# Performance work log

Hardware: AMD Instinct MI355X
Metric: run time of the kernel (lower is better)

## Reference

```python
import jax, jax.numpy as jnp
import numpy as np

S, FRAME, CLS, D, HWA, HWV, DOUT = 32, 8, 32, 512, 8, 14, 128


def setup_inputs() -> dict:
    key = jax.random.key(0)
    ks = jax.random.split(key, 12)
    rng = np.random.default_rng(0)
    # per-(segment,class) random permutation of frames (torch.randperm(frame))
    rand_frames = np.stack([rng.permutation(FRAME) for _ in range(S * CLS)]).reshape(S, CLS, FRAME).astype(np.int32)
    rand_classes = rng.integers(0, CLS, size=(S, CLS, FRAME)).astype(np.int32)
    return {
        "feat_a": jax.random.normal(ks[0], (S * CLS, D, HWA, HWA), jnp.float32),
        "pred_a": jax.random.uniform(ks[1], (S, CLS), jnp.float32),
        "feat_v": jax.random.normal(ks[2], (S * FRAME, D, HWV, HWV), jnp.float32),
        "pred_v": jax.random.normal(ks[3], (S * FRAME, CLS), jnp.float32),
        "cam": jax.random.uniform(ks[4], (S * FRAME, CLS, 1, HWV, HWV), jnp.float32),
        "rand_frames": jnp.asarray(rand_frames),
        "rand_classes": jnp.asarray(rand_classes),
        "Wt": jax.random.normal(ks[5], (D, D), jnp.float32) * (1.0 / np.sqrt(D)),
        "bt": jnp.zeros((D,), jnp.float32),
        "Ws": jax.random.normal(ks[6], (D, D), jnp.float32) * (1.0 / np.sqrt(D)),
        "bs": jnp.zeros((D,), jnp.float32),
        "Wa": jax.random.normal(ks[7], (DOUT, D), jnp.float32) * (1.0 / np.sqrt(D)),
        "ba": jnp.zeros((DOUT,), jnp.float32),
        "Wv": jax.random.normal(ks[8], (DOUT, D), jnp.float32) * (1.0 / np.sqrt(D)),
        "bv": jnp.zeros((DOUT,), jnp.float32),
    }


def reference(feat_a, pred_a, feat_v, pred_v, cam, rand_frames, rand_classes,
              Wt, bt, Ws, bs, Wa, ba, Wv, bv):
    S_, C_ = pred_a.shape
    F_ = pred_v.shape[0] // S_

    # temp_conv (1x1) + AdaptiveMaxPool2d(1,1): max over H,W (bias is per-channel const)
    ca = jnp.einsum('bihw,oi->bohw', feat_a, Wt)  # [S*C, D, H, W]
    fa = ca.max(axis=(2, 3)) + bt                 # [S*C, D]
    fa = fa.reshape(S_, C_, -1)                   # [S, C, D]

    # spa_conv (1x1) then cam-weighted foreground pooling (fg branch of cam_pool)
    cv = jnp.einsum('bihw,oi->bohw', feat_v, Ws) + bs[None, :, None, None]  # [S*F, D, H, W]
    camq = cam[:, :, 0]                                                     # [S*F, C, H, W]
    fg = jnp.einsum('bdhw,bchw->bcd', cv, camq)
    fg = fg / (camq.sum(axis=(2, 3))[..., None] + 1e-10)                    # [S*F, C, D]
    fg = fg.reshape(S_, F_, C_, -1)                                         # [S, F, C, D]

    pv = jax.nn.sigmoid(pred_v.reshape(S_, F_, C_))
    active_a = pred_a > 0.3            # [S, C]  (index_a; the chained-index line is a no-op)
    active_v = pv > 0.3                # [S, F, C] (eff_v membership)

    # transforms
    ta = fa @ Wa.T + ba                                    # [S, C, DOUT]
    tv = jnp.einsum('sfcd,od->sfco', fg, Wv) + bv          # [S, F, C, DOUT]

    # 'same' pairs: (seg, frame, class) where both audio class and video frame-class fire
    mask_co = (active_a[:, None, :] & active_v)            # [S, F, C]
    loss_co = ((ta[:, None, :, :] - tv) ** 2).mean(-1)     # [S, F, C]
    loss_co = jnp.transpose(loss_co, (0, 2, 1)) * jnp.transpose(mask_co, (0, 2, 1))  # [S, C, F]

    # 'differ' pairs: num = int(pred_a*frame) random (frame,class) picks from partner seg
    num = (pred_a * F_).astype(jnp.int32)                  # [S, C]
    mask_di = active_a[:, :, None] & (jnp.arange(F_)[None, None, :] < num[:, :, None])  # [S, C, F]
    rank = jnp.arange(S_) ^ 1                              # seg+1 if even else seg-1
    tv_di = tv[rank[:, None, None], rand_frames, rand_classes]  # [S, C, F, DOUT]
    loss_di = ((ta[:, :, None, :] - tv_di) ** 2).mean(-1) * mask_di  # [S, C, F]

    # dense masked layout of (embed_co, embed_di); invalid slots are exactly 0
    return jnp.stack([loss_co, loss_di])  # [2, S, C, F]
```

## Files before the change

kernel.cpp:

```cpp
#include <hip/hip_runtime.h>


typedef __attribute__((ext_vector_type(8))) short bf16x8;
typedef __attribute__((ext_vector_type(4))) float f32x4;

__device__ __forceinline__ unsigned short f2bf(float x) {
    union { float f; unsigned u; } v; v.f = x;
    unsigned r = v.u + 0x7FFFu + ((v.u >> 16) & 1u);
    return (unsigned short)(r >> 16);
}
__device__ __forceinline__ unsigned pk2(float a, float b) {
    return (unsigned)f2bf(a) | ((unsigned)f2bf(b) << 16);
}

__global__ __launch_bounds__(256) void k0_wtf(
    const float* __restrict__ Wt, unsigned short* __restrict__ WtF)
{
    int g = blockIdx.x * 256 + threadIdx.x;
    int ot = g >> 10, ks = (g >> 6) & 15, l = g & 63;
    int lo = l & 15, hi = l >> 4;
    const float* src = &Wt[(ot*16 + lo) * 512 + ks*32 + hi*8];
    float4 f0 = ((const float4*)src)[0], f1 = ((const float4*)src)[1];
    uint4 u = { pk2(f0.x,f0.y), pk2(f0.z,f0.w), pk2(f1.x,f1.y), pk2(f1.z,f1.w) };
    *(uint4*)&WtF[(size_t)g * 8] = u;
}

__global__ __launch_bounds__(512, 4) void k1_fa(
    const float* __restrict__ feat_a, const unsigned short* __restrict__ WtF,
    const float* __restrict__ bt, float* __restrict__ fa)
{
    __shared__ unsigned short lds_b[64 * 512];
    const int b = blockIdx.x, t = threadIdx.x;
    const int w = t >> 6, l = t & 63, lo = l & 15, hi = l >> 4;

    const float* fb = feat_a + (size_t)b * 32768;
    const int hw = l;
#pragma unroll 2
    for (int it = 0; it < 8; ++it) {
        int koct = it * 8 + w;
        float v[8];
#pragma unroll
        for (int j = 0; j < 8; ++j)
            v[j] = fb[(koct * 8 + j) * 64 + hw];
        unsigned u[4];
#pragma unroll
        for (int j = 0; j < 4; ++j) u[j] = pk2(v[2*j], v[2*j + 1]);
        int chunk = koct ^ (hw & 7);
        *(uint4*)((char*)lds_b + hw * 1024 + chunk * 16) = *(uint4*)u;
    }
    __syncthreads();

    f32x4 acc[4][4];
#pragma unroll
    for (int i = 0; i < 4; ++i)
#pragma unroll
        for (int j = 0; j < 4; ++j) acc[i][j] = (f32x4)(0.f);
    const unsigned short* wtf = WtF + (size_t)(w * 4) * 8192;
    for (int ks = 0; ks < 16; ++ks) {
        bf16x8 bfr[4];
#pragma unroll
        for (int nf = 0; nf < 4; ++nf) {
            int chunk = (ks * 4 + hi) ^ (lo & 7);
            bfr[nf] = *(const bf16x8*)((char*)lds_b + (nf*16 + lo) * 1024 + chunk * 16);
        }
#pragma unroll
        for (int mo = 0; mo < 4; ++mo) {
            bf16x8 afr = *(const bf16x8*)&wtf[(size_t)((mo*16 + ks)*64 + l) * 8];
#pragma unroll
            for (int nf = 0; nf < 4; ++nf)
                acc[mo][nf] = __builtin_amdgcn_mfma_f32_16x16x32_bf16(afr, bfr[nf], acc[mo][nf], 0, 0, 0);
        }
    }
    const int o0 = w * 64;
#pragma unroll
    for (int mo = 0; mo < 4; ++mo)
#pragma unroll
        for (int reg = 0; reg < 4; ++reg) {
            float m = fmaxf(fmaxf(acc[mo][0][reg], acc[mo][1][reg]),
                            fmaxf(acc[mo][2][reg], acc[mo][3][reg]));
            m = fmaxf(m, __shfl_xor(m, 1));
            m = fmaxf(m, __shfl_xor(m, 2));
            m = fmaxf(m, __shfl_xor(m, 4));
            m = fmaxf(m, __shfl_xor(m, 8));
            if (lo == 0) {
                int orow = o0 + mo*16 + hi*4 + reg;
                fa[(size_t)b * 512 + orow] = m + bt[orow];
            }
        }
}

__global__ __launch_bounds__(512) void k2_g(
    const float* __restrict__ feat_v, const float* __restrict__ cam,
    unsigned short* __restrict__ g_bf, float* __restrict__ camsum)
{
    __shared__ unsigned short cam_s[32][232];
    __shared__ unsigned short feat_s[2][64][232];
    const int half = blockIdx.x, b = blockIdx.y, t = threadIdx.x;
    const int w = t >> 6, l = t & 63, lo = l & 15, hi = l >> 4;
    const int mo = w >> 2, nf = w & 3;

    const float* camb = &cam[b * 6272];
    for (int i4 = t; i4 < 1568; i4 += 512) {
        int c = i4 / 49, h4 = (i4 - c*49) * 4;
        float4 v = ((const float4*)camb)[i4];
        *(unsigned*)&cam_s[c][h4]     = pk2(v.x, v.y);
        *(unsigned*)&cam_s[c][h4 + 2] = pk2(v.z, v.w);
    }
    for (int idx = t; idx < 32*28; idx += 512) {
        int c = idx / 28; cam_s[c][196 + (idx - c*28)] = 0;
    }
    for (int idx = t; idx < 2*64*28; idx += 512) {
        int bu = idx / 1792, r = (idx - bu*1792) / 28, hh = 196 + (idx % 28);
        feat_s[bu][r][hh] = 0;
    }
    if (half == 0) {
        int c = t >> 4, seg = l & 15;
        int h0 = seg * 13, h1 = min(196, h0 + 13);
        float s = 0.f;
        const float* p = &camb[c * 196];
        for (int q = h0; q < h1; ++q) s += p[q];
        s += __shfl_xor(s, 1); s += __shfl_xor(s, 2);
        s += __shfl_xor(s, 4); s += __shfl_xor(s, 8);
        if (seg == 0) camsum[b*32 + c] = s;
    }

    auto STAGE = [&](int ic, int bu) {
        const float* fbv = &feat_v[((size_t)b*512 + ic*64) * 196];
        for (int i4 = t; i4 < 3136; i4 += 512) {
            int r = i4 / 49, h4 = (i4 - r*49) * 4;
            float4 v = ((const float4*)fbv)[i4];
            *(unsigned*)&feat_s[bu][r][h4]     = pk2(v.x, v.y);
            *(unsigned*)&feat_s[bu][r][h4 + 2] = pk2(v.z, v.w);
        }
    };
    STAGE(half*4, 0);
    __syncthreads();
    for (int q = 0; q < 4; ++q) {
        int ic = half*4 + q;
        if (q < 3) STAGE(ic + 1, (q + 1) & 1);
        f32x4 acc = (f32x4)(0.f);
#pragma unroll
        for (int kt = 0; kt < 7; ++kt) {
            bf16x8 a  = *(const bf16x8*)&cam_s[mo*16 + lo][kt*32 + hi*8];
            bf16x8 bb = *(const bf16x8*)&feat_s[q & 1][nf*16 + lo][kt*32 + hi*8];
            acc = __builtin_amdgcn_mfma_f32_16x16x32_bf16(a, bb, acc, 0, 0, 0);
        }
#pragma unroll
        for (int reg = 0; reg < 4; ++reg) {
            int c = mo*16 + hi*4 + reg;
            int i = ic*64 + nf*16 + lo;
            g_bf[((size_t)b*32 + c)*512 + i] = f2bf(acc[reg]);
        }
        __syncthreads();
    }
}

__global__ __launch_bounds__(256) void k3_wvs(
    const float* __restrict__ Wv, const float* __restrict__ Ws, const float* __restrict__ bs,
    unsigned short* __restrict__ WvsF, float* __restrict__ wvbs)
{
    __shared__ float red[256];
    const int o = blockIdx.x >> 1, ih = blockIdx.x & 1, t = threadIdx.x;
    const int i = ih*256 + t;
    float a0 = 0.f;
#pragma unroll 4
    for (int d = 0; d < 512; ++d)
        a0 += Wv[o*512 + d] * Ws[d*512 + i];
    int nf = o >> 4, lo2 = o & 15, ks = i >> 5, hi2 = (i >> 3) & 3, j = i & 7;
    WvsF[(size_t)(((nf*16 + ks)*64) + hi2*16 + lo2)*8 + j] = f2bf(a0);
    if (ih == 0) {
        red[t] = Wv[o*512 + t]*bs[t] + Wv[o*512 + t + 256]*bs[t + 256];
        __syncthreads();
        for (int s2 = 128; s2 > 0; s2 >>= 1) {
            if (t < s2) red[t] += red[t + s2];
            __syncthreads();
        }
        if (t == 0) wvbs[o] = red[0];
    }
}

__global__ __launch_bounds__(256) void k4_tv(
    const unsigned short* __restrict__ g_bf, const unsigned short* __restrict__ WvsF,
    const float* __restrict__ camsum, const float* __restrict__ wvbs,
    const float* __restrict__ bv, float* __restrict__ tv)
{
    const int m0 = blockIdx.x * 32;
    const int t = threadIdx.x, w = t >> 6, l = t & 63, lo = l & 15, hi = l >> 4;
    f32x4 acc[2][2];
#pragma unroll
    for (int i = 0; i < 2; ++i)
#pragma unroll
        for (int j = 0; j < 2; ++j) acc[i][j] = (f32x4)(0.f);
    for (int ks = 0; ks < 16; ++ks) {
        bf16x8 a0 = *(const bf16x8*)&g_bf[(size_t)(m0 + lo)*512 + ks*32 + hi*8];
        bf16x8 a1 = *(const bf16x8*)&g_bf[(size_t)(m0 + 16 + lo)*512 + ks*32 + hi*8];
#pragma unroll
        for (int nn = 0; nn < 2; ++nn) {
            int nf = w*2 + nn;
            bf16x8 bb = *(const bf16x8*)&WvsF[(size_t)((nf*16 + ks)*64 + l) * 8];
            acc[0][nn] = __builtin_amdgcn_mfma_f32_16x16x32_bf16(a0, bb, acc[0][nn], 0, 0, 0);
            acc[1][nn] = __builtin_amdgcn_mfma_f32_16x16x32_bf16(a1, bb, acc[1][nn], 0, 0, 0);
        }
    }
#pragma unroll
    for (int mo = 0; mo < 2; ++mo)
#pragma unroll
        for (int reg = 0; reg < 4; ++reg) {
            int bc = m0 + mo*16 + hi*4 + reg;
            float cs = camsum[bc];
            float inv = 1.f / (cs + 1e-10f);
#pragma unroll
            for (int nn = 0; nn < 2; ++nn) {
                int o = (w*2 + nn)*16 + lo;
                tv[(size_t)bc*128 + o] = (acc[mo][nn][reg] + cs * wvbs[o]) * inv + bv[o];
            }
        }
}

__global__ __launch_bounds__(128) void k5_ta(
    const float* __restrict__ fa, const float* __restrict__ Wa,
    const float* __restrict__ ba, float* __restrict__ ta)
{
    __shared__ float fa_s[4 * 512];
    const int r0 = blockIdx.x * 4, t = threadIdx.x;
    for (int j = t; j < 512; j += 128)
        ((float4*)fa_s)[j] = ((const float4*)&fa[r0 * 512])[j];
    __syncthreads();
    float acc[4];
#pragma unroll
    for (int r = 0; r < 4; ++r) acc[r] = 0.f;
    const float4* wa4 = (const float4*)&Wa[t * 512];
#pragma unroll 4
    for (int j = 0; j < 128; ++j) {
        float4 wv = wa4[j];
#pragma unroll
        for (int r = 0; r < 4; ++r) {
            float4 fv = ((const float4*)&fa_s[r * 512])[j];
            acc[r] += wv.x*fv.x + wv.y*fv.y + wv.z*fv.z + wv.w*fv.w;
        }
    }
    float bao = ba[t];
#pragma unroll
    for (int r = 0; r < 4; ++r) ta[(r0 + r)*128 + t] = acc[r] + bao;
}

__global__ __launch_bounds__(256) void k6_loss(
    const float* __restrict__ ta, const float* __restrict__ tv,
    const float* __restrict__ pred_a, const float* __restrict__ pred_v,
    const int* __restrict__ rand_frames, const int* __restrict__ rand_classes,
    float* __restrict__ out)
{
    const int blk = blockIdx.x;
    const int s = blk >> 5, c = blk & 31;
    const int t = threadIdx.x, w = t >> 6, l = t & 63;
    const float ta0 = ta[blk*128 + l], ta1 = ta[blk*128 + 64 + l];
    const float pa = pred_a[blk];
    const bool aa = pa > 0.3f;
    const int num = (int)(pa * 8.0f);
    const float LOGIT03 = -0.84729786f;
#pragma unroll
    for (int ff = 0; ff < 2; ++ff) {
        int f = w*2 + ff;
        int row = (s*8 + f)*32 + c;
        float d0 = ta0 - tv[row*128 + l];
        float d1 = ta1 - tv[row*128 + 64 + l];
        float ss = d0*d0 + d1*d1;
        for (int m = 32; m > 0; m >>= 1) ss += __shfl_xor(ss, m);
        bool av = pred_v[(s*8 + f)*32 + c] > LOGIT03;
        if (l == 0) out[blk*8 + f] = (aa && av) ? ss * (1.f/128.f) : 0.f;
        int fi = rand_frames[blk*8 + f];
        int ci = rand_classes[blk*8 + f];
        int row2 = ((s ^ 1)*8 + fi)*32 + ci;
        float e0 = ta0 - tv[row2*128 + l];
        float e1 = ta1 - tv[row2*128 + 64 + l];
        float s2 = e0*e0 + e1*e1;
        for (int m = 32; m > 0; m >>= 1) s2 += __shfl_xor(s2, m);
        if (l == 0) out[8192 + blk*8 + f] = (aa && (f < num)) ? s2 * (1.f/128.f) : 0.f;
    }
}

extern "C" void kernel_launch(void* const* d_in, const int* in_sizes, int n_in,
                              void* d_out, int out_size, void* d_ws, size_t ws_size,
                              hipStream_t stream) {
    const float* feat_a = (const float*)d_in[0];
    const float* pred_a = (const float*)d_in[1];
    const float* feat_v = (const float*)d_in[2];
    const float* pred_v = (const float*)d_in[3];
    const float* cam    = (const float*)d_in[4];
    const int* rand_frames  = (const int*)d_in[5];
    const int* rand_classes = (const int*)d_in[6];
    const float* Wt = (const float*)d_in[7];
    const float* bt = (const float*)d_in[8];
    const float* Ws = (const float*)d_in[9];
    const float* bs = (const float*)d_in[10];
    const float* Wa = (const float*)d_in[11];
    const float* ba = (const float*)d_in[12];
    const float* Wv = (const float*)d_in[13];
    const float* bv = (const float*)d_in[14];
    float* out = (float*)d_out;

    char* ws = (char*)d_ws;
    float* fa              = (float*)(ws + 0);
    float* ta              = (float*)(ws + 2097152);
    unsigned short* WtF    = (unsigned short*)(ws + 2097152);
    unsigned short* g_bf   = (unsigned short*)(ws + 2621440);
    float* camsum          = (float*)(ws + 11010048);
    unsigned short* WvsF   = (unsigned short*)(ws + 11042816);
    float* wvbs            = (float*)(ws + 11173888);
    float* tv              = (float*)(ws + 11174400);

    k0_wtf<<<128, 256, 0, stream>>>(Wt, WtF);
    k3_wvs<<<256, 256, 0, stream>>>(Wv, Ws, bs, WvsF, wvbs);
    k1_fa<<<1024, 512, 0, stream>>>(feat_a, WtF, bt, fa);
    k2_g<<<dim3(2, 256), 512, 0, stream>>>(feat_v, cam, g_bf, camsum);
    k4_tv<<<256, 256, 0, stream>>>(g_bf, WvsF, camsum, wvbs, bv, tv);
    k5_ta<<<256, 128, 0, stream>>>(fa, Wa, ba, ta);
    k6_loss<<<1024, 256, 0, stream>>>(ta, tv, pred_a, pred_v, rand_frames, rand_classes, out);
}
```

Baseline: 422.8 us.

## Vectorize feat_a loads, double-buffer weight fragments, and halve tv tile rows

In k1_fa, feat_a is now staged into LDS with float4 loads that cover four channels by four pixels, replacing scalar strided loads, and the result is written as 8-byte packed chunks. Weight fragments for the next k-step are prefetched into alternating register buffers so global loads overlap the MFMA work. k4_tv now handles 16 rows per block and launches twice as many blocks for more parallelism, and two scalar loops get a larger unroll factor. These changes raise register pressure, and each k4_tv block loads its weight fragments for half as many rows, so weight traffic doubles.

```diff
diff --git a/kernel.cpp b/kernel.cpp
--- a/kernel.cpp
+++ b/kernel.cpp
@@ -33,20 +33,35 @@
     const int b = blockIdx.x, t = threadIdx.x;
     const int w = t >> 6, l = t & 63, lo = l & 15, hi = l >> 4;
 
-    const float* fb = feat_a + (size_t)b * 32768;
-    const int hw = l;
-#pragma unroll 2
-    for (int it = 0; it < 8; ++it) {
-        int koct = it * 8 + w;
-        float v[8];
-#pragma unroll
-        for (int j = 0; j < 8; ++j)
-            v[j] = fb[(koct * 8 + j) * 64 + hw];
-        unsigned u[4];
-#pragma unroll
-        for (int j = 0; j < 4; ++j) u[j] = pk2(v[2*j], v[2*j + 1]);
-        int chunk = koct ^ (hw & 7);
-        *(uint4*)((char*)lds_b + hw * 1024 + chunk * 16) = *(uint4*)u;
+    const unsigned short* wtf = WtF + (size_t)(w * 4) * 8192;
+
+    bf16x8 afrA[4], afrB[4];
+#pragma unroll
+    for (int mo = 0; mo < 4; ++mo)
+        afrA[mo] = *(const bf16x8*)&wtf[(size_t)((mo*16 + 0)*64 + l) * 8];
+
+    const float4* fb4 = (const float4*)(feat_a + (size_t)b * 32768);
+#pragma unroll
+    for (int it = 0; it < 4; ++it) {
+        int tp = it * 512 + t;
+        int hq = tp & 15, kq = tp >> 4;
+        int hw0 = hq * 4, k0 = kq * 4;
+        float4 v0 = fb4[(k0 + 0) * 16 + hq];
+        float4 v1 = fb4[(k0 + 1) * 16 + hq];
+        float4 v2 = fb4[(k0 + 2) * 16 + hq];
+        float4 v3 = fb4[(k0 + 3) * 16 + hq];
+        int koct = kq >> 1, bo = (kq & 1) * 8;
+        float a0[4] = {v0.x, v0.y, v0.z, v0.w};
+        float a1[4] = {v1.x, v1.y, v1.z, v1.w};
+        float a2[4] = {v2.x, v2.y, v2.z, v2.w};
+        float a3[4] = {v3.x, v3.y, v3.z, v3.w};
+#pragma unroll
+        for (int r = 0; r < 4; ++r) {
+            int hw = hw0 + r;
+            uint2 u = { pk2(a0[r], a1[r]), pk2(a2[r], a3[r]) };
+            int chunk = koct ^ (hw & 7);
+            *(uint2*)((char*)lds_b + hw * 1024 + chunk * 16 + bo) = u;
+        }
     }
     __syncthreads();
 
@@ -55,22 +70,47 @@
     for (int i = 0; i < 4; ++i)
 #pragma unroll
         for (int j = 0; j < 4; ++j) acc[i][j] = (f32x4)(0.f);
-    const unsigned short* wtf = WtF + (size_t)(w * 4) * 8192;
-    for (int ks = 0; ks < 16; ++ks) {
-        bf16x8 bfr[4];
-#pragma unroll
-        for (int nf = 0; nf < 4; ++nf) {
-            int chunk = (ks * 4 + hi) ^ (lo & 7);
-            bfr[nf] = *(const bf16x8*)((char*)lds_b + (nf*16 + lo) * 1024 + chunk * 16);
-        }
-#pragma unroll
-        for (int mo = 0; mo < 4; ++mo) {
-            bf16x8 afr = *(const bf16x8*)&wtf[(size_t)((mo*16 + ks)*64 + l) * 8];
-#pragma unroll
-            for (int nf = 0; nf < 4; ++nf)
-                acc[mo][nf] = __builtin_amdgcn_mfma_f32_16x16x32_bf16(afr, bfr[nf], acc[mo][nf], 0, 0, 0);
-        }
-    }
+
+#pragma unroll
+    for (int ks2 = 0; ks2 < 8; ++ks2) {
+        {
+            const int ks = 2 * ks2;
+#pragma unroll
+            for (int mo = 0; mo < 4; ++mo)
+                afrB[mo] = *(const bf16x8*)&wtf[(size_t)((mo*16 + ks + 1)*64 + l) * 8];
+            bf16x8 bfr[4];
+#pragma unroll
+            for (int nf = 0; nf < 4; ++nf) {
+                int chunk = (ks * 4 + hi) ^ (lo & 7);
+                bfr[nf] = *(const bf16x8*)((char*)lds_b + (nf*16 + lo) * 1024 + chunk * 16);
+            }
+#pragma unroll
+            for (int mo = 0; mo < 4; ++mo)
+#pragma unroll
+                for (int nf = 0; nf < 4; ++nf)
+                    acc[mo][nf] = __builtin_amdgcn_mfma_f32_16x16x32_bf16(afrA[mo], bfr[nf], acc[mo][nf], 0, 0, 0);
+        }
+        {
+            const int ks = 2 * ks2 + 1;
+            if (ks2 < 7) {
+#pragma unroll
+                for (int mo = 0; mo < 4; ++mo)
+                    afrA[mo] = *(const bf16x8*)&wtf[(size_t)((mo*16 + ks + 1)*64 + l) * 8];
+            }
+            bf16x8 bfr[4];
+#pragma unroll
+            for (int nf = 0; nf < 4; ++nf) {
+                int chunk = (ks * 4 + hi) ^ (lo & 7);
+                bfr[nf] = *(const bf16x8*)((char*)lds_b + (nf*16 + lo) * 1024 + chunk * 16);
+            }
+#pragma unroll
+            for (int mo = 0; mo < 4; ++mo)
+#pragma unroll
+                for (int nf = 0; nf < 4; ++nf)
+                    acc[mo][nf] = __builtin_amdgcn_mfma_f32_16x16x32_bf16(afrB[mo], bfr[nf], acc[mo][nf], 0, 0, 0);
+        }
+    }
+
     const int o0 = w * 64;
 #pragma unroll
     for (int mo = 0; mo < 4; ++mo)
@@ -163,7 +203,7 @@
     const int o = blockIdx.x >> 1, ih = blockIdx.x & 1, t = threadIdx.x;
     const int i = ih*256 + t;
     float a0 = 0.f;
-#pragma unroll 4
+#pragma unroll 8
     for (int d = 0; d < 512; ++d)
         a0 += Wv[o*512 + d] * Ws[d*512 + i];
     int nf = o >> 4, lo2 = o & 15, ks = i >> 5, hi2 = (i >> 3) & 3, j = i & 7;
@@ -184,37 +224,30 @@
     const float* __restrict__ camsum, const float* __restrict__ wvbs,
     const float* __restrict__ bv, float* __restrict__ tv)
 {
-    const int m0 = blockIdx.x * 32;
+    const int m0 = blockIdx.x * 16;
     const int t = threadIdx.x, w = t >> 6, l = t & 63, lo = l & 15, hi = l >> 4;
-    f32x4 acc[2][2];
-#pragma unroll
-    for (int i = 0; i < 2; ++i)
-#pragma unroll
-        for (int j = 0; j < 2; ++j) acc[i][j] = (f32x4)(0.f);
+    f32x4 acc[2];
+    acc[0] = (f32x4)(0.f); acc[1] = (f32x4)(0.f);
     for (int ks = 0; ks < 16; ++ks) {
         bf16x8 a0 = *(const bf16x8*)&g_bf[(size_t)(m0 + lo)*512 + ks*32 + hi*8];
-        bf16x8 a1 = *(const bf16x8*)&g_bf[(size_t)(m0 + 16 + lo)*512 + ks*32 + hi*8];
 #pragma unroll
         for (int nn = 0; nn < 2; ++nn) {
             int nf = w*2 + nn;
             bf16x8 bb = *(const bf16x8*)&WvsF[(size_t)((nf*16 + ks)*64 + l) * 8];
-            acc[0][nn] = __builtin_amdgcn_mfma_f32_16x16x32_bf16(a0, bb, acc[0][nn], 0, 0, 0);
-            acc[1][nn] = __builtin_amdgcn_mfma_f32_16x16x32_bf16(a1, bb, acc[1][nn], 0, 0, 0);
-        }
-    }
-#pragma unroll
-    for (int mo = 0; mo < 2; ++mo)
-#pragma unroll
-        for (int reg = 0; reg < 4; ++reg) {
-            int bc = m0 + mo*16 + hi*4 + reg;
-            float cs = camsum[bc];
-            float inv = 1.f / (cs + 1e-10f);
-#pragma unroll
-            for (int nn = 0; nn < 2; ++nn) {
-                int o = (w*2 + nn)*16 + lo;
-                tv[(size_t)bc*128 + o] = (acc[mo][nn][reg] + cs * wvbs[o]) * inv + bv[o];
-            }
-        }
+            acc[nn] = __builtin_amdgcn_mfma_f32_16x16x32_bf16(a0, bb, acc[nn], 0, 0, 0);
+        }
+    }
+#pragma unroll
+    for (int reg = 0; reg < 4; ++reg) {
+        int bc = m0 + hi*4 + reg;
+        float cs = camsum[bc];
+        float inv = 1.f / (cs + 1e-10f);
+#pragma unroll
+        for (int nn = 0; nn < 2; ++nn) {
+            int o = (w*2 + nn)*16 + lo;
+            tv[(size_t)bc*128 + o] = (acc[nn][reg] + cs * wvbs[o]) * inv + bv[o];
+        }
+    }
 }
 
 __global__ __launch_bounds__(128) void k5_ta(
@@ -230,7 +263,7 @@
 #pragma unroll
     for (int r = 0; r < 4; ++r) acc[r] = 0.f;
     const float4* wa4 = (const float4*)&Wa[t * 512];
-#pragma unroll 4
+#pragma unroll 8
     for (int j = 0; j < 128; ++j) {
         float4 wv = wa4[j];
 #pragma unroll
@@ -313,7 +346,7 @@
     k3_wvs<<<256, 256, 0, stream>>>(Wv, Ws, bs, WvsF, wvbs);
     k1_fa<<<1024, 512, 0, stream>>>(feat_a, WtF, bt, fa);
     k2_g<<<dim3(2, 256), 512, 0, stream>>>(feat_v, cam, g_bf, camsum);
-    k4_tv<<<256, 256, 0, stream>>>(g_bf, WvsF, camsum, wvbs, bv, tv);
+    k4_tv<<<512, 256, 0, stream>>>(g_bf, WvsF, camsum, wvbs, bv, tv);
     k5_ta<<<256, 128, 0, stream>>>(fa, Wa, ba, ta);
     k6_loss<<<1024, 256, 0, stream>>>(ta, tv, pred_a, pred_v, rand_frames, rand_classes, out);
 }
```

New measurement: 397.6 us. 6.0% less time.
